# Performance work log

Hardware: AMD Instinct MI355X
Metric: run time of the kernel (lower is better)

## Reference

```python
import jax, jax.numpy as jnp
import numpy as np
import math

HIDDEN = 768
HEADS = 12
HEAD_DIM = HIDDEN // HEADS
B, N = 128, 196
POS = 196


def setup_inputs() -> dict:
    key = jax.random.key(0)
    ks = jax.random.split(key, 12)
    s = 1.0 / math.sqrt(HIDDEN)
    inp = {
        "x": jax.random.normal(ks[0], (B, N, HIDDEN), dtype=jnp.float32),
        "Wq": jax.random.normal(ks[1], (HIDDEN, HIDDEN), dtype=jnp.float32) * s,
        "bq": jnp.zeros((HIDDEN,), dtype=jnp.float32),
        "Wk": jax.random.normal(ks[2], (HIDDEN, HIDDEN), dtype=jnp.float32) * s,
        "bk": jnp.zeros((HIDDEN,), dtype=jnp.float32),
        "Wv": jax.random.normal(ks[3], (HIDDEN, HIDDEN), dtype=jnp.float32) * s,
        "bv": jnp.zeros((HIDDEN,), dtype=jnp.float32),
        "Wp": jax.random.normal(ks[4], (HIDDEN, HIDDEN), dtype=jnp.float32) * s,
        "bp": jnp.zeros((HIDDEN,), dtype=jnp.float32),
        "pos_bias": jax.random.normal(ks[5], (POS, POS), dtype=jnp.float32) * 0.02,
        "mask": jnp.ones((B, 1, 1, N), dtype=jnp.int32),
    }
    return inp


def reference(x, Wq, bq, Wk, bk, Wv, bv, Wp, bp, pos_bias, mask):
    Bx, Nx, C = x.shape
    H, D = HEADS, HEAD_DIM
    # nn.Linear: y = x @ W.T + b
    q = (x @ Wq.T + bq).reshape(Bx, Nx, H, D).transpose(0, 2, 1, 3)  # [B,H,N,D]
    k = (x @ Wk.T + bk).reshape(Bx, Nx, H, D).transpose(0, 2, 1, 3)
    v = (x @ Wv.T + bv).reshape(Bx, Nx, H, D).transpose(0, 2, 1, 3)
    attn = jnp.einsum('bhnd,bhmd->bhnm', q, k) / math.sqrt(D)
    attn = attn + pos_bias[:Nx, :Nx][None, None, :, :]
    attn = jnp.where(mask == 0, -jnp.inf, attn)
    attn = jax.nn.softmax(attn, axis=-1)
    out = jnp.einsum('bhnm,bhmd->bhnd', attn, v)
    out = out.transpose(0, 2, 1, 3).reshape(Bx, Nx, C)
    return out @ Wp.T + bp
```

## Files before the change

### kernel.cpp

```cpp
#include <hip/hip_runtime.h>
#include <hip/hip_bf16.h>

#define HIDDEN 768
#define HEADS 12
#define HEAD_DIM 64
#define BATCH 128
#define SEQ 196
#define M_TOT (BATCH * SEQ)
#define QKV_N (3 * HIDDEN)

typedef __attribute__((ext_vector_type(8))) short bf16x8;
typedef __attribute__((ext_vector_type(8))) unsigned short u16x8;
typedef __attribute__((ext_vector_type(4))) float f32x4;

__device__ __forceinline__ unsigned short f2bf(float f) {
    unsigned int u = __builtin_bit_cast(unsigned int, f);
    unsigned int r = (u + 0x7fffu + ((u >> 16) & 1u)) >> 16;
    return (unsigned short)r;
}

__device__ __forceinline__ ushort4 cvt4(float4 v) {
    ushort4 o;
    o.x = f2bf(v.x); o.y = f2bf(v.y); o.z = f2bf(v.z); o.w = f2bf(v.w);
    return o;
}

__global__ __launch_bounds__(256) void prep_kernel(
    const float* __restrict__ x,
    const float* __restrict__ Wq, const float* __restrict__ Wk,
    const float* __restrict__ Wv, const float* __restrict__ Wp,
    const float* __restrict__ bq, const float* __restrict__ bk,
    const float* __restrict__ bv,
    unsigned short* __restrict__ xb, unsigned short* __restrict__ wqkv,
    unsigned short* __restrict__ wpb, float* __restrict__ biasq)
{
    const long long NX = (long long)M_TOT * HIDDEN / 4;
    const long long NQ = NX + (long long)QKV_N * HIDDEN / 4;
    const long long NP = NQ + (long long)HIDDEN * HIDDEN / 4;
    const long long NB = NP + QKV_N / 4;
    long long tid = (long long)blockIdx.x * 256 + threadIdx.x;
    if (tid < NX) {
        float4 v = ((const float4*)x)[tid];
        ((ushort4*)xb)[tid] = cvt4(v);
    } else if (tid < NQ) {
        int i = (int)(tid - NX);
        int e = i * 4;
        int row = e / HIDDEN, col = e % HIDDEN;
        const float* s = (row < HIDDEN) ? (Wq + (size_t)row * HIDDEN + col)
                       : (row < 2 * HIDDEN) ? (Wk + (size_t)(row - HIDDEN) * HIDDEN + col)
                       : (Wv + (size_t)(row - 2 * HIDDEN) * HIDDEN + col);
        ((ushort4*)wqkv)[i] = cvt4(*(const float4*)s);
    } else if (tid < NP) {
        int i = (int)(tid - NQ);
        ((ushort4*)wpb)[i] = cvt4(((const float4*)Wp)[i]);
    } else if (tid < NB) {
        int i = (int)(tid - NP);
        int e = i * 4;
        const float* s = (e < HIDDEN) ? (bq + e)
                       : (e < 2 * HIDDEN) ? (bk + (e - HIDDEN))
                       : (bv + (e - 2 * HIDDEN));
        *(float4*)(biasq + e) = *(const float4*)s;
    }
}

template <bool OUT_BF16>
__global__ __launch_bounds__(512, 4) void gemm_v4(
    const unsigned short* __restrict__ A,
    const unsigned short* __restrict__ B,
    const float* __restrict__ bias,
    void* __restrict__ C, const int Ncols)
{
    __shared__ __align__(16) unsigned short SMEM[36864];
    const int t = threadIdx.x, w = t >> 6, lane = t & 63;
    const int quad = lane >> 4, l15 = lane & 15;
    const int wm = w >> 2, wn = w & 3;

    const int gx = gridDim.x;
    const int nwg = gx * (int)gridDim.y;
    const int orig = blockIdx.y * gx + blockIdx.x;
    const int qq = nwg >> 3, rr2 = nwg & 7;
    const int xcd = orig & 7, loc = orig >> 3;
    const int wg = (xcd < rr2 ? xcd * (qq + 1) : rr2 * (qq + 1) + (xcd - rr2) * qq) + loc;
    const int m0 = (wg / gx) * 128, n0 = (wg % gx) * 256;

    const int srow = t >> 2, sslot = t & 3;
    const int ksw = (sslot ^ (srow & 3)) << 3;
    const unsigned short* Ag = A + (size_t)(m0 + srow) * HIDDEN + ksw;
    const unsigned short* Bg = B + (size_t)(n0 + srow) * HIDDEN + ksw;
    const int aw = w * 512;
    const int bw = 12288 + w * 512;

#define STAGE(kt2)  do {                                                            \
    __builtin_amdgcn_global_load_lds(                                               \
        (__attribute__((address_space(1))) void*)(Ag + (kt2) * 32),                 \
        (__attribute__((address_space(3))) void*)(SMEM + ((kt2) % 3) * 4096 + aw),  \
        16, 0, 0);                                                                  \
    __builtin_amdgcn_global_load_lds(                                               \
        (__attribute__((address_space(1))) void*)(Bg + (kt2) * 32),                 \
        (__attribute__((address_space(3))) void*)(SMEM + 12288 + ((kt2) % 3) * 8192 + w * 512), \
        16, 0, 0);                                                                  \
    __builtin_amdgcn_global_load_lds(                                               \
        (__attribute__((address_space(1))) void*)(Bg + (size_t)128 * HIDDEN + (kt2) * 32), \
        (__attribute__((address_space(3))) void*)(SMEM + 12288 + ((kt2) % 3) * 8192 + 4096 + w * 512), \
        16, 0, 0);                                                                  \
  } while (0)

    const int fsw = (quad ^ (l15 & 3)) << 3;
    const int aoff = (wm * 64 + l15) * 32 + fsw;
    const int boff = 12288 + (wn * 64 + l15) * 32 + fsw;

    f32x4 acc[4][4] = {};

    STAGE(0);
    STAGE(1);
    asm volatile("s_waitcnt vmcnt(3)" ::: "memory");
    __builtin_amdgcn_s_barrier();

#pragma unroll
    for (int kt = 0; kt < 24; ++kt) {
        const int bufA = (kt % 3) * 4096, bufB = (kt % 3) * 8192;
        if (kt < 22) STAGE(kt + 2);
        bf16x8 Af[4], Bf[4];
#pragma unroll
        for (int i = 0; i < 4; ++i)
            Af[i] = *(const bf16x8*)(SMEM + bufA + aoff + i * 512);
#pragma unroll
        for (int j = 0; j < 4; ++j)
            Bf[j] = *(const bf16x8*)(SMEM + bufB + boff + j * 512);
        asm volatile("s_waitcnt lgkmcnt(0)" ::: "memory");
        __builtin_amdgcn_sched_barrier(0);
        __builtin_amdgcn_s_setprio(1);
#pragma unroll
        for (int i = 0; i < 4; ++i)
#pragma unroll
            for (int j = 0; j < 4; ++j)
                acc[i][j] = __builtin_amdgcn_mfma_f32_16x16x32_bf16(
                    Af[i], Bf[j], acc[i][j], 0, 0, 0);
        __builtin_amdgcn_s_setprio(0);
        __builtin_amdgcn_sched_barrier(0);
        if (kt < 22)       { asm volatile("s_waitcnt vmcnt(3)" ::: "memory"); }
        else if (kt == 22) { asm volatile("s_waitcnt vmcnt(0)" ::: "memory"); }
        if (kt < 23) __builtin_amdgcn_s_barrier();
    }
#undef STAGE

    __syncthreads();
    float* Cs = (float*)SMEM + w * (16 * 68);
    float bvj[4];
#pragma unroll
    for (int j = 0; j < 4; ++j) bvj[j] = bias[n0 + wn * 64 + j * 16 + l15];

#pragma unroll
    for (int i = 0; i < 4; ++i) {
        __builtin_amdgcn_sched_barrier(0);
#pragma unroll
        for (int j = 0; j < 4; ++j)
#pragma unroll
            for (int r = 0; r < 4; ++r)
                Cs[(quad * 4 + r) * 68 + j * 16 + l15] = acc[i][j][r] + bvj[j];
        __builtin_amdgcn_sched_barrier(0);
        asm volatile("s_waitcnt lgkmcnt(0)" ::: "memory");
        if constexpr (OUT_BF16) {
#pragma unroll
            for (int p = 0; p < 2; ++p) {
                const int row = p * 8 + (lane >> 3);
                const int c0 = (lane & 7) * 8;
                float4 a = *(const float4*)&Cs[row * 68 + c0];
                float4 bb = *(const float4*)&Cs[row * 68 + c0 + 4];
                u16x8 pk;
                pk[0] = f2bf(a.x); pk[1] = f2bf(a.y); pk[2] = f2bf(a.z); pk[3] = f2bf(a.w);
                pk[4] = f2bf(bb.x); pk[5] = f2bf(bb.y); pk[6] = f2bf(bb.z); pk[7] = f2bf(bb.w);
                *(u16x8*)((unsigned short*)C +
                          (size_t)(m0 + wm * 64 + i * 16 + row) * Ncols + n0 + wn * 64 + c0) = pk;
            }
        } else {
#pragma unroll
            for (int p = 0; p < 4; ++p) {
                const int row = p * 4 + (lane >> 4);
                const int c0 = (lane & 15) * 4;
                float4 a = *(const float4*)&Cs[row * 68 + c0];
                *(float4*)((float*)C +
                           (size_t)(m0 + wm * 64 + i * 16 + row) * Ncols + n0 + wn * 64 + c0) = a;
            }
        }
        __builtin_amdgcn_sched_barrier(0);
    }
}

__global__ __launch_bounds__(256, 2) void attn_kernel(
    const unsigned short* __restrict__ QKV,
    const float* __restrict__ pos_bias,
    const int* __restrict__ mask,
    unsigned short* __restrict__ ctx)
{
    __shared__ __align__(16) unsigned short Ks[208 * 72];
    __shared__ __align__(16) unsigned short Vt[64 * 256];
    __shared__ __align__(16) unsigned short Os[4][16 * 72];
    const int b = blockIdx.x / HEADS, h = blockIdx.x % HEADS;
    const int t = threadIdx.x, w = t >> 6, lane = t & 63;
    const int quad = lane >> 4, l15 = lane & 15;
    const size_t base = (size_t)b * SEQ * QKV_N + h * HEAD_DIM;

    for (int c = t; c < SEQ * 8; c += 256) {
        int row = c >> 3, d0 = (c & 7) * 8;
        *(bf16x8*)(Ks + row * 72 + d0) =
            *(const bf16x8*)(QKV + base + (size_t)row * QKV_N + HIDDEN + d0);
    }
    {
        bf16x8 z = {};
        for (int i = t; i < 12 * 9; i += 256) {
            int row = 196 + i / 9, d0 = (i % 9) * 8;
            *(bf16x8*)(Ks + row * 72 + d0) = z;
        }
    }
    for (int i = t; i < 64 * 60; i += 256) {
        int row = i / 60, key = 196 + i % 60;
        int s = (row & 7) ^ ((row >> 3) & 7);
        Vt[row * 256 + ((((key >> 3) ^ s) << 3) | (key & 7))] = 0;
    }
    for (int c = t; c < SEQ * 8; c += 256) {
        int key = c >> 3, d0 = (c & 7) * 8;
        bf16x8 vv = *(const bf16x8*)(QKV + base + (size_t)key * QKV_N + 2 * HIDDEN + d0);
        int cb = key >> 3, kk = key & 7;
#pragma unroll
        for (int j = 0; j < 8; ++j) {
            int row = d0 + j;
            int s = (row & 7) ^ ((row >> 3) & 7);
            Vt[row * 256 + (((cb ^ s) << 3) | kk)] = (unsigned short)vv[j];
        }
    }
    __syncthreads();

    int vs[4];
#pragma unroll
    for (int nt = 0; nt < 4; ++nt) {
        int rr = nt * 16 + l15;
        vs[nt] = (rr & 7) ^ ((rr >> 3) & 7);
    }

    for (int t16 = w; t16 < 13; t16 += 4) {
        const int qrow = min(t16 * 16 + l15, SEQ - 1);
        const unsigned short* qp = QKV + base + (size_t)qrow * QKV_N + quad * 8;
        bf16x8 qf0 = *(const bf16x8*)(qp);
        bf16x8 qf1 = *(const bf16x8*)(qp + 32);

        f32x4 accT[13];
#pragma unroll
        for (int jt = 0; jt < 13; ++jt) {
            const unsigned short* kp = Ks + (jt * 16 + l15) * 72 + quad * 8;
            bf16x8 kf0 = *(const bf16x8*)(kp);
            bf16x8 kf1 = *(const bf16x8*)(kp + 32);
            f32x4 z = {};
            z = __builtin_amdgcn_mfma_f32_16x16x32_bf16(kf0, qf0, z, 0, 0, 0);
            z = __builtin_amdgcn_mfma_f32_16x16x32_bf16(kf1, qf1, z, 0, 0, 0);
            accT[jt] = z;
        }

        float mx = -3e38f;
#pragma unroll
        for (int jt = 0; jt < 13; ++jt) {
            const int key0 = jt * 16 + quad * 4;
            const int kb = min(key0, SEQ - 4);
            float4 pb = *(const float4*)(pos_bias + (size_t)qrow * SEQ + kb);
            int4 mk = *(const int4*)(mask + b * SEQ + kb);
#pragma unroll
            for (int r = 0; r < 4; ++r) {
                const int key = key0 + r;
                const bool cv = (key < SEQ) && ((&mk.x)[r] != 0);
                float v = cv ? (accT[jt][r] * 0.125f + (&pb.x)[r]) : -1e30f;
                accT[jt][r] = v;
                mx = fmaxf(mx, v);
            }
        }
        mx = fmaxf(mx, __shfl_xor(mx, 16, 64));
        mx = fmaxf(mx, __shfl_xor(mx, 32, 64));
        float sm = 0.f;
#pragma unroll
        for (int jt = 0; jt < 13; ++jt)
#pragma unroll
            for (int r = 0; r < 4; ++r) {
                float e = __expf(accT[jt][r] - mx);
                accT[jt][r] = e;
                sm += e;
            }
        sm += __shfl_xor(sm, 16, 64);
        sm += __shfl_xor(sm, 32, 64);
        const float inv = 1.0f / sm;

        unsigned int pk[14][2];
#pragma unroll
        for (int jt = 0; jt < 13; ++jt)
#pragma unroll
            for (int pp = 0; pp < 2; ++pp) {
                unsigned int lo = f2bf(accT[jt][2 * pp] * inv);
                unsigned int hi = f2bf(accT[jt][2 * pp + 1] * inv);
                pk[jt][pp] = (hi << 16) | lo;
            }
        pk[13][0] = 0; pk[13][1] = 0;

        f32x4 o[4] = {};
        const int hi_half = quad >> 1;
        const int sq0 = (quad & 1) * 2 * 16 + l15;
        const int sq1 = sq0 + 16;
#pragma unroll
        for (int kt = 0; kt < 7; ++kt) {
            union { unsigned int u[4]; bf16x8 v; } pf;
#pragma unroll
            for (int u = 0; u < 4; ++u) {
                const int src = (u < 2) ? sq0 : sq1;
                unsigned int a0 = (unsigned int)__shfl((int)pk[2 * kt][u & 1], src, 64);
                unsigned int a1 = (unsigned int)__shfl((int)pk[2 * kt + 1][u & 1], src, 64);
                pf.u[u] = hi_half ? a1 : a0;
            }
#pragma unroll
            for (int nt = 0; nt < 4; ++nt) {
                const int rr = nt * 16 + l15;
                const bf16x8 vf = *(const bf16x8*)(
                    &Vt[rr * 256 + (((kt * 4 + quad) ^ vs[nt]) << 3)]);
                o[nt] = __builtin_amdgcn_mfma_f32_16x16x32_bf16(pf.v, vf, o[nt], 0, 0, 0);
            }
        }

        __builtin_amdgcn_sched_barrier(0);
#pragma unroll
        for (int nt = 0; nt < 4; ++nt)
#pragma unroll
            for (int r = 0; r < 4; ++r)
                Os[w][(quad * 4 + r) * 72 + nt * 16 + l15] = f2bf(o[nt][r]);
        __builtin_amdgcn_sched_barrier(0);
        asm volatile("s_waitcnt lgkmcnt(0)" ::: "memory");
#pragma unroll
        for (int p = 0; p < 2; ++p) {
            const int row = p * 8 + (lane >> 3);
            const int grow = t16 * 16 + row;
            const int c0 = (lane & 7) * 8;
            bf16x8 ov = *(const bf16x8*)&Os[w][row * 72 + c0];
            if (grow < SEQ)
                *(bf16x8*)(ctx + ((size_t)b * SEQ + grow) * HIDDEN + h * HEAD_DIM + c0) = ov;
        }
        __builtin_amdgcn_sched_barrier(0);
    }
}

extern "C" void kernel_launch(void* const* d_in, const int* in_sizes, int n_in,
                              void* d_out, int out_size, void* d_ws, size_t ws_size,
                              hipStream_t stream) {
    const float* x    = (const float*)d_in[0];
    const float* Wq   = (const float*)d_in[1];
    const float* bq   = (const float*)d_in[2];
    const float* Wk   = (const float*)d_in[3];
    const float* bk   = (const float*)d_in[4];
    const float* Wv   = (const float*)d_in[5];
    const float* bv   = (const float*)d_in[6];
    const float* Wp   = (const float*)d_in[7];
    const float* bp   = (const float*)d_in[8];
    const float* pos  = (const float*)d_in[9];
    const int*   mask = (const int*)d_in[10];

    char* ws = (char*)d_ws;
    size_t off = 0;
    auto alloc = [&](size_t bytes) -> char* {
        char* p = ws + off;
        off += (bytes + 255) & ~(size_t)255;
        return p;
    };
    unsigned short* xb    = (unsigned short*)alloc((size_t)M_TOT * HIDDEN * 2);
    unsigned short* wqkv  = (unsigned short*)alloc((size_t)QKV_N * HIDDEN * 2);
    unsigned short* wpb   = (unsigned short*)alloc((size_t)HIDDEN * HIDDEN * 2);
    float*          biasq = (float*)alloc((size_t)QKV_N * 4);
    unsigned short* qkv   = (unsigned short*)alloc((size_t)M_TOT * QKV_N * 2);
    unsigned short* ctx   = (unsigned short*)alloc((size_t)M_TOT * HIDDEN * 2);

    prep_kernel<<<21123, 256, 0, stream>>>(x, Wq, Wk, Wv, Wp, bq, bk, bv,
                                           xb, wqkv, wpb, biasq);
    gemm_v4<true><<<dim3(QKV_N / 256, M_TOT / 128), 512, 0, stream>>>(
        xb, wqkv, biasq, (void*)qkv, QKV_N);
    attn_kernel<<<BATCH * HEADS, 256, 0, stream>>>(qkv, pos, mask, ctx);
    gemm_v4<false><<<dim3(HIDDEN / 256, M_TOT / 128), 512, 0, stream>>>(
        ctx, wpb, bp, d_out, HIDDEN);
}
```

Before: 363.4 us.

## Software-pipeline LDS fragment loads with MFMAs and deepen GEMM prefetch

Rewrites the GEMM main loop so the LDS fragment reads for the next k-tile are interleaved between MFMA groups of the current tile, using double-buffered A fragment registers. It adds a third global-to-LDS prefetch stage, merges the A and B buffers into one layout per stage, and changes the LDS swizzle to XOR with row>>1 to reduce bank conflicts. The goal is to hide LDS latency behind matrix math and keep more memory traffic in flight. In exchange it needs more registers, which risks lower occupancy, and the hand-ordered waitcnt and barrier placement is fragile.

```diff
diff --git a/kernel.cpp b/kernel.cpp
--- a/kernel.cpp
+++ b/kernel.cpp
@@ -64,7 +64,7 @@
 }
 
 template <bool OUT_BF16>
-__global__ __launch_bounds__(512, 4) void gemm_v4(
+__global__ __launch_bounds__(512, 4) void gemm_v6(
     const unsigned short* __restrict__ A,
     const unsigned short* __restrict__ B,
     const float* __restrict__ bias,
@@ -84,65 +84,114 @@
     const int m0 = (wg / gx) * 128, n0 = (wg % gx) * 256;
 
     const int srow = t >> 2, sslot = t & 3;
-    const int ksw = (sslot ^ (srow & 3)) << 3;
+    const int ksw = (sslot ^ ((srow >> 1) & 3)) << 3;
     const unsigned short* Ag = A + (size_t)(m0 + srow) * HIDDEN + ksw;
     const unsigned short* Bg = B + (size_t)(n0 + srow) * HIDDEN + ksw;
-    const int aw = w * 512;
-    const int bw = 12288 + w * 512;
-
-#define STAGE(kt2)  do {                                                            \
+
+#define GLLDS(srcp, dsto)                                                           \
     __builtin_amdgcn_global_load_lds(                                               \
-        (__attribute__((address_space(1))) void*)(Ag + (kt2) * 32),                 \
-        (__attribute__((address_space(3))) void*)(SMEM + ((kt2) % 3) * 4096 + aw),  \
-        16, 0, 0);                                                                  \
-    __builtin_amdgcn_global_load_lds(                                               \
-        (__attribute__((address_space(1))) void*)(Bg + (kt2) * 32),                 \
-        (__attribute__((address_space(3))) void*)(SMEM + 12288 + ((kt2) % 3) * 8192 + w * 512), \
-        16, 0, 0);                                                                  \
-    __builtin_amdgcn_global_load_lds(                                               \
-        (__attribute__((address_space(1))) void*)(Bg + (size_t)128 * HIDDEN + (kt2) * 32), \
-        (__attribute__((address_space(3))) void*)(SMEM + 12288 + ((kt2) % 3) * 8192 + 4096 + w * 512), \
-        16, 0, 0);                                                                  \
+        (__attribute__((address_space(1))) void*)(srcp),                            \
+        (__attribute__((address_space(3))) void*)(SMEM + (dsto)), 16, 0, 0)
+
+#define STAGE3(tt, bb) do {                                                         \
+    GLLDS(Ag + (tt) * 32,          (bb) * 12288 +        w * 512);                  \
+    GLLDS(Bg + (tt) * 32,          (bb) * 12288 + 4096 + w * 512);                  \
+    GLLDS(Bg + 98304 + (tt) * 32,  (bb) * 12288 + 8192 + w * 512);                  \
   } while (0)
 
-    const int fsw = (quad ^ (l15 & 3)) << 3;
+    const int fsw = (quad ^ ((l15 >> 1) & 3)) << 3;
     const int aoff = (wm * 64 + l15) * 32 + fsw;
-    const int boff = 12288 + (wn * 64 + l15) * 32 + fsw;
+    const int boff = 4096 + (wn * 64 + l15) * 32 + fsw;
 
     f32x4 acc[4][4] = {};
-
-    STAGE(0);
-    STAGE(1);
+    bf16x8 AfA[4], AfB[4], Bf[4];
+
+#define MF(a, b, c) __builtin_amdgcn_mfma_f32_16x16x32_bf16(a, b, c, 0, 0, 0)
+
+    STAGE3(0, 0);
+    STAGE3(1, 1);
+    STAGE3(2, 2);
     asm volatile("s_waitcnt vmcnt(3)" ::: "memory");
     __builtin_amdgcn_s_barrier();
-
-#pragma unroll
-    for (int kt = 0; kt < 24; ++kt) {
-        const int bufA = (kt % 3) * 4096, bufB = (kt % 3) * 8192;
-        if (kt < 22) STAGE(kt + 2);
-        bf16x8 Af[4], Bf[4];
-#pragma unroll
-        for (int i = 0; i < 4; ++i)
-            Af[i] = *(const bf16x8*)(SMEM + bufA + aoff + i * 512);
-#pragma unroll
-        for (int j = 0; j < 4; ++j)
-            Bf[j] = *(const bf16x8*)(SMEM + bufB + boff + j * 512);
-        asm volatile("s_waitcnt lgkmcnt(0)" ::: "memory");
-        __builtin_amdgcn_sched_barrier(0);
-        __builtin_amdgcn_s_setprio(1);
-#pragma unroll
-        for (int i = 0; i < 4; ++i)
-#pragma unroll
-            for (int j = 0; j < 4; ++j)
-                acc[i][j] = __builtin_amdgcn_mfma_f32_16x16x32_bf16(
-                    Af[i], Bf[j], acc[i][j], 0, 0, 0);
-        __builtin_amdgcn_s_setprio(0);
-        __builtin_amdgcn_sched_barrier(0);
-        if (kt < 22)       { asm volatile("s_waitcnt vmcnt(3)" ::: "memory"); }
-        else if (kt == 22) { asm volatile("s_waitcnt vmcnt(0)" ::: "memory"); }
-        if (kt < 23) __builtin_amdgcn_s_barrier();
-    }
-#undef STAGE
+#pragma unroll
+    for (int i = 0; i < 4; ++i)
+        AfA[i] = *(const bf16x8*)(SMEM + aoff + i * 512);
+#pragma unroll
+    for (int j = 0; j < 4; ++j)
+        Bf[j] = *(const bf16x8*)(SMEM + boff + j * 512);
+    asm volatile("s_waitcnt lgkmcnt(0)" ::: "memory");
+    __builtin_amdgcn_s_barrier();
+
+#define TILE(kt, CUR, NXT, DOS, DON, ENDW) do {                                     \
+    if (DOS) STAGE3((kt) + 3, (kt) % 3);                                            \
+    __builtin_amdgcn_sched_barrier(0);                                              \
+    acc[0][0] = MF(CUR[0], Bf[0], acc[0][0]);                                       \
+    acc[1][0] = MF(CUR[1], Bf[0], acc[1][0]);                                       \
+    acc[2][0] = MF(CUR[2], Bf[0], acc[2][0]);                                       \
+    acc[3][0] = MF(CUR[3], Bf[0], acc[3][0]);                                       \
+    __builtin_amdgcn_sched_barrier(0);                                              \
+    if (DON) {                                                                      \
+        Bf[0]  = *(const bf16x8*)(SMEM + (((kt)+1)%3)*12288 + boff + 0*512);        \
+        NXT[0] = *(const bf16x8*)(SMEM + (((kt)+1)%3)*12288 + aoff + 0*512);        \
+    }                                                                               \
+    __builtin_amdgcn_sched_barrier(0);                                              \
+    acc[0][1] = MF(CUR[0], Bf[1], acc[0][1]);                                       \
+    acc[1][1] = MF(CUR[1], Bf[1], acc[1][1]);                                       \
+    acc[2][1] = MF(CUR[2], Bf[1], acc[2][1]);                                       \
+    acc[3][1] = MF(CUR[3], Bf[1], acc[3][1]);                                       \
+    __builtin_amdgcn_sched_barrier(0);                                              \
+    if (DON) {                                                                      \
+        Bf[1]  = *(const bf16x8*)(SMEM + (((kt)+1)%3)*12288 + boff + 1*512);        \
+        NXT[1] = *(const bf16x8*)(SMEM + (((kt)+1)%3)*12288 + aoff + 1*512);        \
+    }                                                                               \
+    __builtin_amdgcn_sched_barrier(0);                                              \
+    acc[0][2] = MF(CUR[0], Bf[2], acc[0][2]);                                       \
+    acc[1][2] = MF(CUR[1], Bf[2], acc[1][2]);                                       \
+    acc[2][2] = MF(CUR[2], Bf[2], acc[2][2]);                                       \
+    acc[3][2] = MF(CUR[3], Bf[2], acc[3][2]);                                       \
+    __builtin_amdgcn_sched_barrier(0);                                              \
+    if (DON) {                                                                      \
+        Bf[2]  = *(const bf16x8*)(SMEM + (((kt)+1)%3)*12288 + boff + 2*512);        \
+        NXT[2] = *(const bf16x8*)(SMEM + (((kt)+1)%3)*12288 + aoff + 2*512);        \
+    }                                                                               \
+    __builtin_amdgcn_sched_barrier(0);                                              \
+    acc[0][3] = MF(CUR[0], Bf[3], acc[0][3]);                                       \
+    acc[1][3] = MF(CUR[1], Bf[3], acc[1][3]);                                       \
+    acc[2][3] = MF(CUR[2], Bf[3], acc[2][3]);                                       \
+    acc[3][3] = MF(CUR[3], Bf[3], acc[3][3]);                                       \
+    __builtin_amdgcn_sched_barrier(0);                                              \
+    if (DON) {                                                                      \
+        Bf[3]  = *(const bf16x8*)(SMEM + (((kt)+1)%3)*12288 + boff + 3*512);        \
+        NXT[3] = *(const bf16x8*)(SMEM + (((kt)+1)%3)*12288 + aoff + 3*512);        \
+    }                                                                               \
+    if (ENDW == 1) {                                                                \
+        asm volatile("s_waitcnt vmcnt(3) lgkmcnt(0)" ::: "memory");                 \
+        __builtin_amdgcn_s_barrier();                                               \
+    } else if (ENDW == 2) {                                                         \
+        asm volatile("s_waitcnt vmcnt(0) lgkmcnt(0)" ::: "memory");                 \
+        __builtin_amdgcn_s_barrier();                                               \
+    }                                                                               \
+    __builtin_amdgcn_sched_barrier(0);                                              \
+  } while (0)
+
+    TILE( 0, AfA, AfB, 1, 1, 1);  TILE( 1, AfB, AfA, 1, 1, 1);
+    TILE( 2, AfA, AfB, 1, 1, 1);  TILE( 3, AfB, AfA, 1, 1, 1);
+    TILE( 4, AfA, AfB, 1, 1, 1);  TILE( 5, AfB, AfA, 1, 1, 1);
+    TILE( 6, AfA, AfB, 1, 1, 1);  TILE( 7, AfB, AfA, 1, 1, 1);
+    TILE( 8, AfA, AfB, 1, 1, 1);  TILE( 9, AfB, AfA, 1, 1, 1);
+    TILE(10, AfA, AfB, 1, 1, 1);  TILE(11, AfB, AfA, 1, 1, 1);
+    TILE(12, AfA, AfB, 1, 1, 1);  TILE(13, AfB, AfA, 1, 1, 1);
+    TILE(14, AfA, AfB, 1, 1, 1);  TILE(15, AfB, AfA, 1, 1, 1);
+    TILE(16, AfA, AfB, 1, 1, 1);  TILE(17, AfB, AfA, 1, 1, 1);
+    TILE(18, AfA, AfB, 1, 1, 1);  TILE(19, AfB, AfA, 1, 1, 1);
+    TILE(20, AfA, AfB, 1, 1, 1);
+    TILE(21, AfB, AfA, 0, 1, 2);
+    TILE(22, AfA, AfB, 0, 1, 0);
+    TILE(23, AfB, AfA, 0, 0, 0);
+#undef TILE
+#undef STAGE3
+#undef GLLDS
+#undef MF
 
     __syncthreads();
     float* Cs = (float*)SMEM + w * (16 * 68);
@@ -373,9 +422,9 @@
 
     prep_kernel<<<21123, 256, 0, stream>>>(x, Wq, Wk, Wv, Wp, bq, bk, bv,
                                            xb, wqkv, wpb, biasq);
-    gemm_v4<true><<<dim3(QKV_N / 256, M_TOT / 128), 512, 0, stream>>>(
+    gemm_v6<true><<<dim3(QKV_N / 256, M_TOT / 128), 512, 0, stream>>>(
         xb, wqkv, biasq, (void*)qkv, QKV_N);
     attn_kernel<<<BATCH * HEADS, 256, 0, stream>>>(qkv, pos, mask, ctx);
-    gemm_v4<false><<<dim3(HIDDEN / 256, M_TOT / 128), 512, 0, stream>>>(
+    gemm_v6<false><<<dim3(HIDDEN / 256, M_TOT / 128), 512, 0, stream>>>(
         ctx, wpb, bp, d_out, HIDDEN);
 }
```

New measurement: 370.4 us. No clear change (+1.9%).
